# Kernel tuning notes

Measured on AMD Instinct MI355X. Metric: run time of the kernel, lower is better.

Reference implementation:

```python
import jax, jax.numpy as jnp
import numpy as np

DEPTH = 3
UNITS = 512
INNER = 32          # inner_dim == F-1
F = INNER + 1
B, N = 128, 100


def setup_inputs() -> dict:
    key = jax.random.key(0)
    k1, k2, k3, k4, k5 = jax.random.split(key, 5)
    x = jax.random.normal(k1, (B, N, N, F), dtype=jnp.float32)
    # W_inner: identity tiled + small uniform noise (init_inner='identity')
    W_inner = (jnp.tile(jnp.eye(INNER, dtype=jnp.float32)[None], (DEPTH + 1, 1, 1))
               + jax.random.uniform(k2, (DEPTH + 1, INNER, INNER), minval=-0.05, maxval=0.05))
    b_inner = jax.random.uniform(k3, (DEPTH + 1, 1, INNER), minval=-0.05, maxval=0.05)
    # W_output: uniform with scale_output=0.01, tiled across depths; b_output zeros
    W_out_single = jax.random.uniform(k4, (INNER, UNITS), minval=-0.01, maxval=0.01)
    W_output = jnp.tile(W_out_single[None], (DEPTH + 1, 1, 1))
    b_output = jnp.zeros((DEPTH + 1, 1, UNITS), dtype=jnp.float32)
    return {"x": x, "W_inner": W_inner, "b_inner": b_inner,
            "W_output": W_output, "b_output": b_output}


def _fp_contribution(attr, W_output, b_output, d):
    # softmax over the units axis, per atom; attr[:, :-1] is [N, INNER]
    return jax.nn.softmax(attr[:, :-1] @ W_output[d] + b_output[d, 0], axis=-1)


def _single(graph0, W_inner, b_inner, W_output, b_output):
    # graph0: [N, N, F]
    attr = jnp.diagonal(graph0, axis1=0, axis2=1).T            # [N, F]
    fp = _fp_contribution(attr, W_output, b_output, 0).sum(axis=0)
    bonds = graph0[:, :, -1]                                    # [N, N]
    boa_T = (bonds + jnp.eye(bonds.shape[0], dtype=graph0.dtype)).T  # bonds_or_atoms transposed: [i,j]=boa[j,i]
    graph = graph0
    for d in range(1, DEPTH + 1):
        pre = graph.sum(axis=1)                                 # [N, F] row-sums of each feature slice
        core = pre[:, :-1] @ W_inner[d] + b_inner[d, 0]         # linear inner activation
        new_attr = jnp.concatenate([core, attr[:, -1:]], axis=1)  # keep bond channel
        # graph[i,j,f] += boa[j,i] * (new_attr - attr)[i,f]  (rank-1 per atom)
        graph = graph + boa_T[:, :, None] * (new_attr - attr)[:, None, :]
        attr = new_attr
        fp = fp + _fp_contribution(attr, W_output, b_output, d).sum(axis=0)
    return fp


def reference(x, W_inner, b_inner, W_output, b_output):
    return jax.vmap(lambda g: _single(g, W_inner, b_inner, W_output, b_output))(x)  # [B, UNITS]
```

## Files before the change

### kernel.cpp

```cpp
#include <hip/hip_runtime.h>

typedef __attribute__((ext_vector_type(4))) float f32x4;
typedef __attribute__((ext_vector_type(8))) short s16x8;

#define NB 128
#define NA 100
#define KF 32
#define NF 33
#define NU 512
#define ND 3

#define SZ_S0    (NB * NA * KF)
#define SZ_BONDS (NB * NA * NA)

__device__ __forceinline__ unsigned short f2bf(float f) {
    unsigned int u = __float_as_uint(f);
    u = (u + 0x7fffu + ((u >> 16) & 1u)) >> 16;
    return (unsigned short)u;
}
__device__ __forceinline__ float bf2f(unsigned short h) {
    return __uint_as_float(((unsigned int)h) << 16);
}

__global__ __launch_bounds__(256) void p1_reduce(const float* __restrict__ x,
    float* __restrict__ S0, float* __restrict__ attrAll, float* __restrict__ bonds)
{
    const int blk = blockIdx.x;
    const int b   = blk / NA;
    const int i   = blk % NA;
    const int t   = threadIdx.x;

    __shared__ float lds[NA * NF];
    __shared__ float red[8][KF];

    const float4* row4 = (const float4*)(x + (size_t)blk * (NA * NF));
    float4* lds4 = (float4*)lds;
    for (int idx = t; idx < (NA * NF) / 4; idx += 256) lds4[idx] = row4[idx];
    __syncthreads();

    const int g = t >> 5;
    const int f = t & 31;
    float p0 = 0.f, p1 = 0.f;
    for (int j = g; j + 8 < NA; j += 16) {
        p0 += lds[j * NF + f];
        p1 += lds[(j + 8) * NF + f];
    }
    if (g < 4) p0 += lds[(96 + g) * NF + f];
    red[g][f] = p0 + p1;
    __syncthreads();

    if (t < KF) {
        float s = 0.f;
#pragma unroll
        for (int gg = 0; gg < 8; ++gg) s += red[gg][t];
        S0[(size_t)blk * KF + t] = s;
    } else if (t >= 64 && t < 64 + KF) {
        attrAll[(size_t)b * (ND + 1) * NA * KF + (size_t)i * KF + (t - 64)] = lds[i * NF + (t - 64)];
    } else if (t >= 128 && t < 128 + NA) {
        const int j = t - 128;
        bonds[(size_t)blk * NA + j] = lds[j * NF + KF];
    }
}

#define NAH 50
#define ELH (NAH * KF)
__global__ __launch_bounds__(256) void p2a_recur(
    const float* __restrict__ S0, const float* __restrict__ bonds,
    const float* __restrict__ W_inner, const float* __restrict__ b_inner,
    float* __restrict__ attrAll,
    const float* __restrict__ W_output,
    unsigned short* __restrict__ WBh, unsigned short* __restrict__ WBl)
{
    const int blk = blockIdx.x;
    const int t   = threadIdx.x;

    if (blk >= NB * 2) {
        const int base = (blk - NB * 2) * 4096;
        for (int j = t; j < 4096; j += 256) {
            const int i = base + j;
            const int d = i >> 14, rem = i & 16383, k = rem >> 9, col = rem & 511;
            const float v = W_output[(size_t)d * (KF * NU) + (size_t)k * NU + col];
            const unsigned short hi = f2bf(v);
            const unsigned short lo = f2bf(v - bf2f(hi));
            const int dst = d * 16384 + (col >> 4) * 512 + (k >> 3) * 128 + (col & 15) * 8 + (k & 7);
            WBh[dst] = hi;
            WBl[dst] = lo;
        }
        return;
    }

    __shared__ float S[ELH];
    __shared__ float attr[ELH];
    __shared__ float rs[NAH];

    const int half = blk & 1;
    const int b    = blk >> 1;
    const int f    = t & 31;

    const float4* s4 = (const float4*)(S0 + (size_t)b * NA * KF + half * ELH);
    const float4* a4 = (const float4*)(attrAll + (size_t)b * (ND + 1) * NA * KF + half * ELH);
    for (int idx = t; idx < ELH / 4; idx += 256) {
        ((float4*)S)[idx]    = s4[idx];
        ((float4*)attr)[idx] = a4[idx];
    }
    if (t < NAH) {
        const int i = half * NAH + t;
        const float* bb = bonds + (size_t)b * NA * NA + i;
        float c0=0.f,c1=0.f,c2=0.f,c3=0.f,c4=0.f,c5=0.f,c6=0.f,c7=0.f;
        int j = 0;
        for (; j + 8 <= NA; j += 8) {
            c0 += bb[(j+0)*NA]; c1 += bb[(j+1)*NA];
            c2 += bb[(j+2)*NA]; c3 += bb[(j+3)*NA];
            c4 += bb[(j+4)*NA]; c5 += bb[(j+5)*NA];
            c6 += bb[(j+6)*NA]; c7 += bb[(j+7)*NA];
        }
        for (; j < NA; ++j) c0 += bb[j*NA];
        rs[t] = 1.f + (((c0+c1)+(c2+c3))+((c4+c5)+(c6+c7)));
    }
    __syncthreads();

    float* attrDst = attrAll + (size_t)b * (ND + 1) * NA * KF + half * ELH;

    for (int d = 1; d <= ND; ++d) {
        float Wc[KF];
        const float* Wd = W_inner + d * KF * KF + f;
#pragma unroll
        for (int k = 0; k < KF; ++k) Wc[k] = Wd[k * KF];
        const float bi = b_inner[d * KF + f];

        float core[7];
#pragma unroll
        for (int it = 0; it < 7; ++it) {
            const int idx = t + it * 256;
            if (idx < ELH) {
                const int row = idx >> 5;
                const float4* Sr4 = (const float4*)(S + row * KF);
                float acc = bi;
#pragma unroll
                for (int q = 0; q < 8; ++q) {
                    const float4 sv = Sr4[q];
                    acc += sv.x * Wc[4*q] + sv.y * Wc[4*q+1]
                         + sv.z * Wc[4*q+2] + sv.w * Wc[4*q+3];
                }
                core[it] = acc;
            }
        }
        __syncthreads();
#pragma unroll
        for (int it = 0; it < 7; ++it) {
            const int idx = t + it * 256;
            if (idx < ELH) {
                const int row = idx >> 5;
                const float cc  = core[it];
                const float old = attr[idx];
                attr[idx] = cc;
                S[idx] += rs[row] * (cc - old);
                attrDst[(size_t)d * NA * KF + idx] = cc;
            }
        }
        __syncthreads();
    }
}

__global__ __launch_bounds__(448, 4) void p2b_mfma(
    const float* __restrict__ attrAll,
    const unsigned short* __restrict__ WBh_g, const unsigned short* __restrict__ WBl_g,
    const float* __restrict__ b_output, float* __restrict__ fpPart)
{
    extern __shared__ unsigned char smraw[];
    unsigned short* WBh  = (unsigned short*)smraw;
    unsigned short* WBl  = WBh + 16384;
    unsigned short* aAh  = WBl + 16384;
    unsigned short* aAl  = aAh + 3584;
    float*          biasL= (float*)(aAl + 3584);
    float*          fpw  = (float*)aAh;

    const int blk = blockIdx.x;
    const int b   = blk & (NB - 1);
    const int d   = blk >> 7;
    const int t   = threadIdx.x;
    const int l   = t & 63;
    const int w   = t >> 6;

    for (int i = t; i < 2048; i += 448) ((float4*)WBh)[i] = ((const float4*)WBh_g)[d * 2048 + i];
    for (int i = t; i < 2048; i += 448) ((float4*)WBl)[i] = ((const float4*)WBl_g)[d * 2048 + i];
    for (int i = t; i < NU; i += 448)   biasL[i] = b_output[d * NU + i];

    const float* A = attrAll + ((size_t)b * (ND + 1) + d) * (NA * KF);
    for (int i = t; i < 3584; i += 448) {
        const int gr = i >> 5, k = i & 31;
        const float v = (gr < NA) ? A[gr * KF + k] : 0.f;
        const unsigned short hi = f2bf(v);
        const unsigned short lo = f2bf(v - bf2f(hi));
        const int dst = ((gr >> 4) * 4 + (k >> 3)) * 128 + (gr & 15) * 8 + (k & 7);
        aAh[dst] = hi;
        aAl[dst] = lo;
    }
    __syncthreads();

    const int aoff = (w * 4 + (l >> 4)) * 128 + (l & 15) * 8;
    const s16x8 ah = *(const s16x8*)&aAh[aoff];
    const s16x8 al = *(const s16x8*)&aAl[aoff];
    __syncthreads();

    const int laneoff = (l >> 4) * 128 + (l & 15) * 8;
    const f32x4 z = {0.f, 0.f, 0.f, 0.f};

    float m[4] = {-1e30f, -1e30f, -1e30f, -1e30f};
#pragma unroll 4
    for (int tt = 0; tt < 32; ++tt) {
        const s16x8 bh = *(const s16x8*)&WBh[tt * 512 + laneoff];
        const f32x4 c = __builtin_amdgcn_mfma_f32_16x16x32_bf16(ah, bh, z, 0, 0, 0);
        const float bias = biasL[tt * 16 + (l & 15)];
#pragma unroll
        for (int r = 0; r < 4; ++r) m[r] = fmaxf(m[r], c[r] + bias);
    }
#pragma unroll
    for (int off = 1; off <= 8; off <<= 1)
#pragma unroll
        for (int r = 0; r < 4; ++r) m[r] = fmaxf(m[r], __shfl_xor(m[r], off, 64));

    float s[4] = {0.f, 0.f, 0.f, 0.f};
#pragma unroll 2
    for (int tt = 0; tt < 32; ++tt) {
        const s16x8 bh = *(const s16x8*)&WBh[tt * 512 + laneoff];
        const s16x8 bl = *(const s16x8*)&WBl[tt * 512 + laneoff];
        const f32x4 c1 = __builtin_amdgcn_mfma_f32_16x16x32_bf16(ah, bh, z, 0, 0, 0);
        const f32x4 c2 = __builtin_amdgcn_mfma_f32_16x16x32_bf16(ah, bl, z, 0, 0, 0);
        const f32x4 c3 = __builtin_amdgcn_mfma_f32_16x16x32_bf16(al, bh, z, 0, 0, 0);
        const float bias = biasL[tt * 16 + (l & 15)];
#pragma unroll
        for (int r = 0; r < 4; ++r) {
            const float cv = ((c1[r] + c2[r]) + c3[r]) + bias;
            s[r] += __expf(cv - m[r]);
        }
    }
#pragma unroll
    for (int off = 1; off <= 8; off <<= 1)
#pragma unroll
        for (int r = 0; r < 4; ++r) s[r] += __shfl_xor(s[r], off, 64);

    float K[4];
#pragma unroll
    for (int r = 0; r < 4; ++r) {
        const int grow = w * 16 + (l >> 4) * 4 + r;
        K[r] = (grow < NA) ? (m[r] + __logf(s[r])) : 1e30f;
    }

#pragma unroll 2
    for (int tt = 0; tt < 32; ++tt) {
        const s16x8 bh = *(const s16x8*)&WBh[tt * 512 + laneoff];
        const s16x8 bl = *(const s16x8*)&WBl[tt * 512 + laneoff];
        const f32x4 c1 = __builtin_amdgcn_mfma_f32_16x16x32_bf16(ah, bh, z, 0, 0, 0);
        const f32x4 c2 = __builtin_amdgcn_mfma_f32_16x16x32_bf16(ah, bl, z, 0, 0, 0);
        const f32x4 c3 = __builtin_amdgcn_mfma_f32_16x16x32_bf16(al, bh, z, 0, 0, 0);
        const float bias = biasL[tt * 16 + (l & 15)];
        float f = 0.f;
#pragma unroll
        for (int r = 0; r < 4; ++r)
            f += __expf(((c1[r] + c2[r]) + c3[r]) + bias - K[r]);
        f += __shfl_xor(f, 16, 64);
        f += __shfl_xor(f, 32, 64);
        if (l < 16) fpw[w * NU + tt * 16 + l] = f;
    }
    __syncthreads();

    for (int u = t; u < NU; u += 448) {
        float sacc = 0.f;
#pragma unroll
        for (int ww = 0; ww < 7; ++ww) sacc += fpw[ww * NU + u];
        fpPart[((size_t)d * NB + b) * NU + u] = sacc;
    }
}

__global__ __launch_bounds__(512) void p2c_out(const float* __restrict__ fpPart,
                                               float* __restrict__ out)
{
    const int b = blockIdx.x, t = threadIdx.x;
    float s = 0.f;
#pragma unroll
    for (int d = 0; d <= ND; ++d) s += fpPart[((size_t)d * NB + b) * NU + t];
    out[(size_t)b * NU + t] = s;
}

extern "C" void kernel_launch(void* const* d_in, const int* in_sizes, int n_in,
                              void* d_out, int out_size, void* d_ws, size_t ws_size,
                              hipStream_t stream) {
    (void)in_sizes; (void)n_in; (void)out_size; (void)ws_size;
    const float* x        = (const float*)d_in[0];
    const float* W_inner  = (const float*)d_in[1];
    const float* b_inner  = (const float*)d_in[2];
    const float* W_output = (const float*)d_in[3];
    const float* b_output = (const float*)d_in[4];
    float* out = (float*)d_out;

    float* S0      = (float*)d_ws;
    float* bonds   = S0 + SZ_S0;
    float* attrAll = bonds + SZ_BONDS;
    float* fpPart  = bonds;
    unsigned short* WBh = (unsigned short*)(attrAll + (size_t)NB * (ND + 1) * NA * KF);
    unsigned short* WBl = WBh + 65536;

    p1_reduce<<<NB * NA, 256, 0, stream>>>(x, S0, attrAll, bonds);
    p2a_recur<<<NB * 2 + 16, 256, 0, stream>>>(S0, bonds, W_inner, b_inner, attrAll,
                                               W_output, WBh, WBl);

    const size_t smemB = 81920;
    hipFuncSetAttribute(reinterpret_cast<const void*>(p2b_mfma),
                        hipFuncAttributeMaxDynamicSharedMemorySize, (int)smemB);
    p2b_mfma<<<NB * (ND + 1), 448, smemB, stream>>>(attrAll, WBh, WBl, b_output, fpPart);
    p2c_out<<<NB, 512, 0, stream>>>(fpPart, out);
}
```

Baseline: 74.07 us.

## Pre-pack attr MFMA fragments upstream, cache half the exps, fuse final reduction

Producers now write the attr hi/lo bf16 MFMA fragments straight to global, so p2b loads A operands directly and no longer converts them in LDS. Weights and bias are pre-scaled by log2(e) so exp2/log2 intrinsics replace expf/logf. The three MFMAs now chain into one accumulator. Exponentials for the second half of the units are cached as packed bf16 in registers and rescaled by 1/sum instead of being recomputed, which adds rounding error and register pressure. The separate output kernel is replaced by a last-block-wins atomic counter inside p2b.

Result: slower. 139.2 us (+87.9%).

```diff
diff --git a/kernel.cpp b/kernel.cpp
--- a/kernel.cpp
+++ b/kernel.cpp
@@ -9,9 +9,14 @@
 #define NF 33
 #define NU 512
 #define ND 3
+#define LOG2E 1.4426950408889634f
 
 #define SZ_S0    (NB * NA * KF)
 #define SZ_BONDS (NB * NA * NA)
+#define FRAG_PER_BD 3584
+
+#define EXP2F(x) __builtin_amdgcn_exp2f(x)
+#define LOG2F(x) __builtin_amdgcn_logf(x)
 
 __device__ __forceinline__ unsigned short f2bf(float f) {
     unsigned int u = __float_as_uint(f);
@@ -21,9 +26,18 @@
 __device__ __forceinline__ float bf2f(unsigned short h) {
     return __uint_as_float(((unsigned int)h) << 16);
 }
+__device__ __forceinline__ unsigned int pack_bf16(float a, float b) {
+    const unsigned int ua = (__float_as_uint(a) + 0x8000u) >> 16;
+    const unsigned int ub = (__float_as_uint(b) + 0x8000u) & 0xffff0000u;
+    return ua | ub;
+}
+__device__ __forceinline__ int frag_idx(int gr, int k) {
+    return ((gr >> 4) * 4 + (k >> 3)) * 128 + (gr & 15) * 8 + (k & 7);
+}
 
 __global__ __launch_bounds__(256) void p1_reduce(const float* __restrict__ x,
-    float* __restrict__ S0, float* __restrict__ attrAll, float* __restrict__ bonds)
+    float* __restrict__ S0, float* __restrict__ attr0f, float* __restrict__ bonds,
+    unsigned short* __restrict__ aFH, unsigned short* __restrict__ aFL)
 {
     const int blk = blockIdx.x;
     const int b   = blk / NA;
@@ -55,7 +69,14 @@
         for (int gg = 0; gg < 8; ++gg) s += red[gg][t];
         S0[(size_t)blk * KF + t] = s;
     } else if (t >= 64 && t < 64 + KF) {
-        attrAll[(size_t)b * (ND + 1) * NA * KF + (size_t)i * KF + (t - 64)] = lds[i * NF + (t - 64)];
+        const int k = t - 64;
+        const float v = lds[i * NF + k];
+        attr0f[(size_t)blk * KF + k] = v;
+        const unsigned short hi = f2bf(v);
+        const unsigned short lo = f2bf(v - bf2f(hi));
+        const size_t base = (size_t)(b * 4 + 0) * FRAG_PER_BD + frag_idx(i, k);
+        aFH[base] = hi;
+        aFL[base] = lo;
     } else if (t >= 128 && t < 128 + NA) {
         const int j = t - 128;
         bonds[(size_t)blk * NA + j] = lds[j * NF + KF];
@@ -67,25 +88,36 @@
 __global__ __launch_bounds__(256) void p2a_recur(
     const float* __restrict__ S0, const float* __restrict__ bonds,
     const float* __restrict__ W_inner, const float* __restrict__ b_inner,
-    float* __restrict__ attrAll,
+    const float* __restrict__ attr0f,
     const float* __restrict__ W_output,
-    unsigned short* __restrict__ WBh, unsigned short* __restrict__ WBl)
+    unsigned short* __restrict__ WBh, unsigned short* __restrict__ WBl,
+    unsigned short* __restrict__ aFH, unsigned short* __restrict__ aFL,
+    int* __restrict__ cnt)
 {
     const int blk = blockIdx.x;
     const int t   = threadIdx.x;
 
     if (blk >= NB * 2) {
-        const int base = (blk - NB * 2) * 4096;
+        const int pb = blk - NB * 2;
+        if (pb == 0 && t < NB) cnt[t] = 0;
+        const int base = pb * 4096;
         for (int j = t; j < 4096; j += 256) {
             const int i = base + j;
             const int d = i >> 14, rem = i & 16383, k = rem >> 9, col = rem & 511;
-            const float v = W_output[(size_t)d * (KF * NU) + (size_t)k * NU + col];
+            const float v = W_output[(size_t)d * (KF * NU) + (size_t)k * NU + col] * LOG2E;
             const unsigned short hi = f2bf(v);
             const unsigned short lo = f2bf(v - bf2f(hi));
             const int dst = d * 16384 + (col >> 4) * 512 + (k >> 3) * 128 + (col & 15) * 8 + (k & 7);
             WBh[dst] = hi;
             WBl[dst] = lo;
         }
+        for (int e = pb * 12288 + t; e < (pb + 1) * 12288; e += 256) {
+            const int bd = e / 384, r = e % 384;
+            const int kg = r / 96, r2 = r % 96, row = r2 >> 3, k = r2 & 7;
+            const size_t dst = (size_t)bd * FRAG_PER_BD + 3072 + kg * 128 + (4 + row) * 8 + k;
+            aFH[dst] = 0;
+            aFL[dst] = 0;
+        }
         return;
     }
 
@@ -98,7 +130,7 @@
     const int f    = t & 31;
 
     const float4* s4 = (const float4*)(S0 + (size_t)b * NA * KF + half * ELH);
-    const float4* a4 = (const float4*)(attrAll + (size_t)b * (ND + 1) * NA * KF + half * ELH);
+    const float4* a4 = (const float4*)(attr0f + (size_t)b * NA * KF + half * ELH);
     for (int idx = t; idx < ELH / 4; idx += 256) {
         ((float4*)S)[idx]    = s4[idx];
         ((float4*)attr)[idx] = a4[idx];
@@ -119,8 +151,6 @@
     }
     __syncthreads();
 
-    float* attrDst = attrAll + (size_t)b * (ND + 1) * NA * KF + half * ELH;
-
     for (int d = 1; d <= ND; ++d) {
         float Wc[KF];
         const float* Wd = W_inner + d * KF * KF + f;
@@ -155,7 +185,12 @@
                 const float old = attr[idx];
                 attr[idx] = cc;
                 S[idx] += rs[row] * (cc - old);
-                attrDst[(size_t)d * NA * KF + idx] = cc;
+                const int gr = half * NAH + row;
+                const unsigned short hi = f2bf(cc);
+                const unsigned short lo = f2bf(cc - bf2f(hi));
+                const size_t base = (size_t)(b * 4 + d) * FRAG_PER_BD + frag_idx(gr, idx & 31);
+                aFH[base] = hi;
+                aFL[base] = lo;
             }
         }
         __syncthreads();
@@ -163,17 +198,17 @@
 }
 
 __global__ __launch_bounds__(448, 4) void p2b_mfma(
-    const float* __restrict__ attrAll,
+    const unsigned short* __restrict__ aFH, const unsigned short* __restrict__ aFL,
     const unsigned short* __restrict__ WBh_g, const unsigned short* __restrict__ WBl_g,
-    const float* __restrict__ b_output, float* __restrict__ fpPart)
+    const float* __restrict__ b_output, float* __restrict__ fpPart,
+    int* __restrict__ cnt, float* __restrict__ out)
 {
     extern __shared__ unsigned char smraw[];
     unsigned short* WBh  = (unsigned short*)smraw;
     unsigned short* WBl  = WBh + 16384;
-    unsigned short* aAh  = WBl + 16384;
-    unsigned short* aAl  = aAh + 3584;
-    float*          biasL= (float*)(aAl + 3584);
-    float*          fpw  = (float*)aAh;
+    float*          biasL= (float*)(WBl + 16384);
+    float*          fpw  = biasL + NU;
+    __shared__ int win;
 
     const int blk = blockIdx.x;
     const int b   = blk & (NB - 1);
@@ -184,23 +219,11 @@
 
     for (int i = t; i < 2048; i += 448) ((float4*)WBh)[i] = ((const float4*)WBh_g)[d * 2048 + i];
     for (int i = t; i < 2048; i += 448) ((float4*)WBl)[i] = ((const float4*)WBl_g)[d * 2048 + i];
-    for (int i = t; i < NU; i += 448)   biasL[i] = b_output[d * NU + i];
-
-    const float* A = attrAll + ((size_t)b * (ND + 1) + d) * (NA * KF);
-    for (int i = t; i < 3584; i += 448) {
-        const int gr = i >> 5, k = i & 31;
-        const float v = (gr < NA) ? A[gr * KF + k] : 0.f;
-        const unsigned short hi = f2bf(v);
-        const unsigned short lo = f2bf(v - bf2f(hi));
-        const int dst = ((gr >> 4) * 4 + (k >> 3)) * 128 + (gr & 15) * 8 + (k & 7);
-        aAh[dst] = hi;
-        aAl[dst] = lo;
-    }
-    __syncthreads();
-
-    const int aoff = (w * 4 + (l >> 4)) * 128 + (l & 15) * 8;
-    const s16x8 ah = *(const s16x8*)&aAh[aoff];
-    const s16x8 al = *(const s16x8*)&aAl[aoff];
+    for (int i = t; i < NU; i += 448)   biasL[i] = b_output[d * NU + i] * LOG2E;
+
+    const size_t abase = (size_t)(b * 4 + d) * FRAG_PER_BD + (w * 4 + (l >> 4)) * 128 + (l & 15) * 8;
+    const s16x8 ah = *(const s16x8*)&aFH[abase];
+    const s16x8 al = *(const s16x8*)&aFL[abase];
     __syncthreads();
 
     const int laneoff = (l >> 4) * 128 + (l & 15) * 8;
@@ -222,47 +245,77 @@
 
     float s[4] = {0.f, 0.f, 0.f, 0.f};
 #pragma unroll 2
-    for (int tt = 0; tt < 32; ++tt) {
+    for (int tt = 0; tt < 16; ++tt) {
         const s16x8 bh = *(const s16x8*)&WBh[tt * 512 + laneoff];
         const s16x8 bl = *(const s16x8*)&WBl[tt * 512 + laneoff];
-        const f32x4 c1 = __builtin_amdgcn_mfma_f32_16x16x32_bf16(ah, bh, z, 0, 0, 0);
-        const f32x4 c2 = __builtin_amdgcn_mfma_f32_16x16x32_bf16(ah, bl, z, 0, 0, 0);
-        const f32x4 c3 = __builtin_amdgcn_mfma_f32_16x16x32_bf16(al, bh, z, 0, 0, 0);
+        f32x4 c = __builtin_amdgcn_mfma_f32_16x16x32_bf16(ah, bh, z, 0, 0, 0);
+        c = __builtin_amdgcn_mfma_f32_16x16x32_bf16(ah, bl, c, 0, 0, 0);
+        c = __builtin_amdgcn_mfma_f32_16x16x32_bf16(al, bh, c, 0, 0, 0);
         const float bias = biasL[tt * 16 + (l & 15)];
 #pragma unroll
-        for (int r = 0; r < 4; ++r) {
-            const float cv = ((c1[r] + c2[r]) + c3[r]) + bias;
-            s[r] += __expf(cv - m[r]);
-        }
+        for (int r = 0; r < 4; ++r)
+            s[r] += EXP2F(c[r] + bias - m[r]);
+    }
+
+    unsigned int eP[32];
+#pragma unroll
+    for (int tt = 16; tt < 32; ++tt) {
+        const s16x8 bh = *(const s16x8*)&WBh[tt * 512 + laneoff];
+        const s16x8 bl = *(const s16x8*)&WBl[tt * 512 + laneoff];
+        f32x4 c = __builtin_amdgcn_mfma_f32_16x16x32_bf16(ah, bh, z, 0, 0, 0);
+        c = __builtin_amdgcn_mfma_f32_16x16x32_bf16(ah, bl, c, 0, 0, 0);
+        c = __builtin_amdgcn_mfma_f32_16x16x32_bf16(al, bh, c, 0, 0, 0);
+        const float bias = biasL[tt * 16 + (l & 15)];
+        const float e0 = EXP2F(c[0] + bias - m[0]);
+        const float e1 = EXP2F(c[1] + bias - m[1]);
+        const float e2 = EXP2F(c[2] + bias - m[2]);
+        const float e3 = EXP2F(c[3] + bias - m[3]);
+        s[0] += e0; s[1] += e1; s[2] += e2; s[3] += e3;
+        eP[(tt - 16) * 2]     = pack_bf16(e0, e1);
+        eP[(tt - 16) * 2 + 1] = pack_bf16(e2, e3);
     }
 #pragma unroll
     for (int off = 1; off <= 8; off <<= 1)
 #pragma unroll
         for (int r = 0; r < 4; ++r) s[r] += __shfl_xor(s[r], off, 64);
 
-    float K[4];
+    float K[4], inv[4];
 #pragma unroll
     for (int r = 0; r < 4; ++r) {
         const int grow = w * 16 + (l >> 4) * 4 + r;
-        K[r] = (grow < NA) ? (m[r] + __logf(s[r])) : 1e30f;
+        const bool ok = (grow < NA);
+        K[r]   = ok ? (m[r] + LOG2F(s[r])) : 1e30f;
+        inv[r] = ok ? (1.f / s[r]) : 0.f;
     }
 
 #pragma unroll 2
-    for (int tt = 0; tt < 32; ++tt) {
+    for (int tt = 0; tt < 16; ++tt) {
         const s16x8 bh = *(const s16x8*)&WBh[tt * 512 + laneoff];
         const s16x8 bl = *(const s16x8*)&WBl[tt * 512 + laneoff];
-        const f32x4 c1 = __builtin_amdgcn_mfma_f32_16x16x32_bf16(ah, bh, z, 0, 0, 0);
-        const f32x4 c2 = __builtin_amdgcn_mfma_f32_16x16x32_bf16(ah, bl, z, 0, 0, 0);
-        const f32x4 c3 = __builtin_amdgcn_mfma_f32_16x16x32_bf16(al, bh, z, 0, 0, 0);
+        f32x4 c = __builtin_amdgcn_mfma_f32_16x16x32_bf16(ah, bh, z, 0, 0, 0);
+        c = __builtin_amdgcn_mfma_f32_16x16x32_bf16(ah, bl, c, 0, 0, 0);
+        c = __builtin_amdgcn_mfma_f32_16x16x32_bf16(al, bh, c, 0, 0, 0);
         const float bias = biasL[tt * 16 + (l & 15)];
         float f = 0.f;
 #pragma unroll
         for (int r = 0; r < 4; ++r)
-            f += __expf(((c1[r] + c2[r]) + c3[r]) + bias - K[r]);
+            f += EXP2F(c[r] + bias - K[r]);
         f += __shfl_xor(f, 16, 64);
         f += __shfl_xor(f, 32, 64);
         if (l < 16) fpw[w * NU + tt * 16 + l] = f;
     }
+#pragma unroll
+    for (int tt = 16; tt < 32; ++tt) {
+        const unsigned int p01 = eP[(tt - 16) * 2];
+        const unsigned int p23 = eP[(tt - 16) * 2 + 1];
+        float f = __uint_as_float(p01 << 16)         * inv[0]
+                + __uint_as_float(p01 & 0xffff0000u) * inv[1]
+                + __uint_as_float(p23 << 16)         * inv[2]
+                + __uint_as_float(p23 & 0xffff0000u) * inv[3];
+        f += __shfl_xor(f, 16, 64);
+        f += __shfl_xor(f, 32, 64);
+        if (l < 16) fpw[w * NU + tt * 16 + l] = f;
+    }
     __syncthreads();
 
     for (int u = t; u < NU; u += 448) {
@@ -271,16 +324,23 @@
         for (int ww = 0; ww < 7; ++ww) sacc += fpw[ww * NU + u];
         fpPart[((size_t)d * NB + b) * NU + u] = sacc;
     }
-}
-
-__global__ __launch_bounds__(512) void p2c_out(const float* __restrict__ fpPart,
-                                               float* __restrict__ out)
-{
-    const int b = blockIdx.x, t = threadIdx.x;
-    float s = 0.f;
-#pragma unroll
-    for (int d = 0; d <= ND; ++d) s += fpPart[((size_t)d * NB + b) * NU + t];
-    out[(size_t)b * NU + t] = s;
+
+    __syncthreads();
+    if (t == 0) {
+        __threadfence();
+        win = (atomicAdd(&cnt[b], 1) == 3);
+    }
+    __syncthreads();
+    if (win) {
+        __threadfence();
+        volatile const float* fp = fpPart;
+        for (int u = t; u < NU; u += 448) {
+            out[(size_t)b * NU + u] = fp[(0 * NB + b) * NU + u]
+                                    + fp[(1 * NB + b) * NU + u]
+                                    + fp[(2 * NB + b) * NU + u]
+                                    + fp[(3 * NB + b) * NU + u];
+        }
+    }
 }
 
 extern "C" void kernel_launch(void* const* d_in, const int* in_sizes, int n_in,
@@ -296,18 +356,21 @@
 
     float* S0      = (float*)d_ws;
     float* bonds   = S0 + SZ_S0;
-    float* attrAll = bonds + SZ_BONDS;
-    float* fpPart  = bonds;
-    unsigned short* WBh = (unsigned short*)(attrAll + (size_t)NB * (ND + 1) * NA * KF);
+    float* attr0f  = bonds + SZ_BONDS;
+    unsigned short* aFH = (unsigned short*)(attr0f + SZ_S0);
+    unsigned short* aFL = aFH + (size_t)NB * 4 * FRAG_PER_BD;
+    unsigned short* WBh = aFL + (size_t)NB * 4 * FRAG_PER_BD;
     unsigned short* WBl = WBh + 65536;
-
-    p1_reduce<<<NB * NA, 256, 0, stream>>>(x, S0, attrAll, bonds);
-    p2a_recur<<<NB * 2 + 16, 256, 0, stream>>>(S0, bonds, W_inner, b_inner, attrAll,
-                                               W_output, WBh, WBl);
+    int* cnt = (int*)(WBl + 65536);
+    float* fpPart = bonds;
+
+    p1_reduce<<<NB * NA, 256, 0, stream>>>(x, S0, attr0f, bonds, aFH, aFL);
+    p2a_recur<<<NB * 2 + 16, 256, 0, stream>>>(S0, bonds, W_inner, b_inner, attr0f,
+                                               W_output, WBh, WBl, aFH, aFL, cnt);
 
     const size_t smemB = 81920;
     hipFuncSetAttribute(reinterpret_cast<const void*>(p2b_mfma),
                         hipFuncAttributeMaxDynamicSharedMemorySize, (int)smemB);
-    p2b_mfma<<<NB * (ND + 1), 448, smemB, stream>>>(attrAll, WBh, WBl, b_output, fpPart);
-    p2c_out<<<NB, 512, 0, stream>>>(fpPart, out);
-}
+    p2b_mfma<<<NB * (ND + 1), 448, smemB, stream>>>(aFH, aFL, WBh, WBl, b_output,
+                                                    fpPart, cnt, out);
+}
```
